# Performance work log

Hardware: AMD Instinct MI355X
Metric: run time of the kernel (lower is better)

## Reference

```python
import jax, jax.numpy as jnp
import numpy as np

NUM_HEADS = 8


def setup_inputs() -> dict:
    key = jax.random.key(0)
    ks = jax.random.split(key, 5)
    B, C, H, W = 2, 256, 64, 64
    # 0.02 scaling keeps logits in a sane range so softmax is not one-hot
    return {
        "x": jax.random.normal(ks[0], (B, C, H, W), dtype=jnp.float32),
        "w_qkv": jax.random.normal(ks[1], (3 * C, C), dtype=jnp.float32) * 0.02,
        "b_qkv": jax.random.normal(ks[2], (3 * C,), dtype=jnp.float32) * 0.02,
        "w_proj": jax.random.normal(ks[3], (C, C), dtype=jnp.float32) * 0.02,
        "b_proj": jax.random.normal(ks[4], (C,), dtype=jnp.float32) * 0.02,
    }


def reference(x, w_qkv, b_qkv, w_proj, b_proj):
    B, C, H, W = x.shape
    N = H * W
    h = NUM_HEADS
    d = C // h
    # 1x1 conv == per-pixel linear: (B,C,H,W) -> (B,3C,H,W)
    qkv = jnp.einsum('oc,bchw->bohw', w_qkv, x) + b_qkv[None, :, None, None]
    qkv = qkv.reshape(B, 3, h, d, N)
    # q,k,v: (B, h, N, d)
    q = jnp.swapaxes(qkv[:, 0], -2, -1)
    k = jnp.swapaxes(qkv[:, 1], -2, -1)
    v = jnp.swapaxes(qkv[:, 2], -2, -1)
    scale = d ** (-0.5)
    attn = jax.nn.softmax(jnp.einsum('bhnd,bhmd->bhnm', q, k) * scale, axis=-1)
    out = jnp.einsum('bhnm,bhmd->bhnd', attn, v)  # (B, h, N, d)
    # faithful to torch: transpose(1,2) -> (B,N,h,d), then row-major reshape to (B,C,H,W)
    out = jnp.swapaxes(out, 1, 2).reshape(B, C, H, W)
    out = jnp.einsum('oc,bchw->bohw', w_proj, out) + b_proj[None, :, None, None]
    return out
```

## Files before the change

### kernel.cpp

```cpp
#include <hip/hip_runtime.h>
#include <hip/hip_bf16.h>


typedef __bf16 bf16;
typedef __bf16 bf16x4 __attribute__((ext_vector_type(4)));
typedef __bf16 bf16x8 __attribute__((ext_vector_type(8)));
typedef float  f32x4  __attribute__((ext_vector_type(4)));
typedef short  s16x4  __attribute__((ext_vector_type(4)));

#if __has_builtin(__builtin_amdgcn_mfma_f32_16x16x16bf16_1k)
#define HAVE_MFMA16 1
#endif

#if __has_builtin(__builtin_amdgcn_exp2f)
#define EXP2(x) __builtin_amdgcn_exp2f(x)
#else
#define EXP2(x) exp2f(x)
#endif

#define NS 4096
#define QSCALE (0.17677669529663687f * 1.4426950408889634f)

static __device__ inline unsigned pack2(float a, float b) {
  union { bf16 h[2]; unsigned u; } v;
  v.h[0] = (bf16)a; v.h[1] = (bf16)b;
  return v.u;
}

__global__ __launch_bounds__(256) void qkv_fused(
    const float* __restrict__ x, const float* __restrict__ w,
    const float* __restrict__ bias,
    bf16* __restrict__ qbuf, bf16* __restrict__ kbuf, bf16* __restrict__ vbuf)
{
  __shared__ bf16 As[64 * 264];
  __shared__ bf16 Bs[64 * 264];
  const int n0 = blockIdx.x * 64, o0 = blockIdx.y * 64, b = blockIdx.z;
  const int t = threadIdx.x;
  const int wv = t >> 6, L = t & 63, quad = L >> 4, lb = L & 15;

  {
    unsigned* A32 = (unsigned*)As;
    const int nj = (t & 15) * 4;
#pragma unroll
    for (int p = 0; p < 8; p++) {
      const int c = p * 32 + (t >> 4) * 2;
      const float* xr = x + ((size_t)(b * 256 + c)) * NS + n0 + nj;
      f32x4 va = *(const f32x4*)xr;
      f32x4 vb = *(const f32x4*)(xr + NS);
#pragma unroll
      for (int i = 0; i < 4; i++)
        A32[(nj + i) * 132 + (c >> 1)] = pack2(va[i], vb[i]);
    }
  }
  {
    const int cj = (t & 15) * 16;
#pragma unroll
    for (int p = 0; p < 4; p++) {
      const int r = p * 16 + (t >> 4);
      const float* wr = w + (size_t)(o0 + r) * 256 + cj;
      f32x4 w0 = *(const f32x4*)wr,       w1 = *(const f32x4*)(wr + 4);
      f32x4 w2 = *(const f32x4*)(wr + 8), w3 = *(const f32x4*)(wr + 12);
      bf16x8 lo, hi;
#pragma unroll
      for (int i = 0; i < 4; i++) {
        lo[i] = (bf16)w0[i]; lo[4 + i] = (bf16)w1[i];
        hi[i] = (bf16)w2[i]; hi[4 + i] = (bf16)w3[i];
      }
      *(bf16x8*)&Bs[r * 264 + cj] = lo;
      *(bf16x8*)&Bs[r * 264 + cj + 8] = hi;
    }
  }
  __syncthreads();

  f32x4 acc[4] = {};
#pragma unroll
  for (int ks = 0; ks < 8; ks++) {
    const bf16x8 bfr = *(const bf16x8*)&Bs[(wv * 16 + lb) * 264 + ks * 32 + quad * 8];
#pragma unroll
    for (int a = 0; a < 4; a++) {
      const bf16x8 afr = *(const bf16x8*)&As[(a * 16 + lb) * 264 + ks * 32 + quad * 8];
      acc[a] = __builtin_amdgcn_mfma_f32_16x16x32_bf16(afr, bfr, acc[a], 0, 0, 0);
    }
  }

  const int comp = o0 >> 8;
  const int o = o0 + wv * 16 + lb;
  const float bv = bias[o];
  if (comp < 2) {
    bf16* dst = (comp == 0) ? qbuf : kbuf;
    const float sc = (comp == 0) ? QSCALE : 1.0f;
    const int hh = (o & 255) >> 5, dd = o & 31;
    const size_t base = ((size_t)b * 8 + hh) * NS;
#pragma unroll
    for (int a = 0; a < 4; a++)
#pragma unroll
      for (int r = 0; r < 4; r++) {
        const int n = n0 + a * 16 + quad * 4 + r;
        dst[(base + n) * 32 + dd] = (bf16)((acc[a][r] + bv) * sc);
      }
  } else {
    __syncthreads();
    bf16* Vt2 = As;
#pragma unroll
    for (int a = 0; a < 4; a++)
#pragma unroll
      for (int r = 0; r < 4; r++)
        Vt2[(wv * 16 + lb) * 72 + a * 16 + quad * 4 + r] = (bf16)(acc[a][r] + bv);
    __syncthreads();
    const int row = t & 63;
    const int o2 = o0 + row;
    const int hh2 = (o2 & 255) >> 5, dd2 = o2 & 31;
    const int hc = (t >> 6) * 16;
    bf16x8 v0 = *(const bf16x8*)&Vt2[row * 72 + hc];
    bf16x8 v1 = *(const bf16x8*)&Vt2[row * 72 + hc + 8];
    bf16* vd = vbuf + (((size_t)b * 8 + hh2) * 32 + dd2) * NS + n0 + hc;
    *(bf16x8*)vd = v0;
    *(bf16x8*)(vd + 8) = v1;
  }
}

__global__ __launch_bounds__(256) void attn_kernel(
    const bf16* __restrict__ qbuf, const bf16* __restrict__ kbuf,
    const bf16* __restrict__ vbuf, bf16* __restrict__ abuf)
{
  __shared__ bf16 Ks[2][64 * 40];
  __shared__ bf16 Vts[2][32 * 80];
#ifndef HAVE_MFMA16
  __shared__ bf16 Ps[4][16 * 72];
#endif

  const int qb = blockIdx.x;
  const int bh = blockIdx.y;
  const bf16* Q  = qbuf + (size_t)bh * NS * 32;
  const bf16* K  = kbuf + (size_t)bh * NS * 32;
  const bf16* Vt = vbuf + (size_t)bh * 32 * NS;

  const int t = threadIdx.x;
  const int wv = t >> 6, L = t & 63, quad = L >> 4, lb = L & 15;
  const int qrow = qb * 64 + wv * 16;

  const bf16x8 qfrag = *(const bf16x8*)(Q + (size_t)(qrow + lb) * 32 + quad * 8);

  const int ki = t >> 2, kj = (t & 3) * 8;
  const int vr = t >> 3, vc = (t & 7) * 8;
  const bf16* Kg = K + (size_t)ki * 32 + kj;
  const bf16* Vg = Vt + (size_t)vr * NS + vc;

  bf16x8 kreg = *(const bf16x8*)Kg;
  bf16x8 vreg = *(const bf16x8*)Vg;

  f32x4 oacc0 = {0.f, 0.f, 0.f, 0.f};
  f32x4 oacc1 = {0.f, 0.f, 0.f, 0.f};
  f32x4 oacc2 = {0.f, 0.f, 0.f, 0.f};
  const f32x4 zero4 = {0.f, 0.f, 0.f, 0.f};
#ifdef HAVE_MFMA16
  const s16x4 ones = {(short)0x3F80, (short)0x3F80, (short)0x3F80, (short)0x3F80};
#else
  float l_i = 0.f;
#endif

#pragma unroll 2
  for (int kt = 0; kt < 64; kt++) {
    const int buf = kt & 1;
    *(bf16x8*)&Ks[buf][ki * 40 + kj] = kreg;
    *(bf16x8*)&Vts[buf][vr * 80 + vc] = vreg;
    __syncthreads();
    if (kt < 63) {
      kreg = *(const bf16x8*)(Kg + (size_t)(kt + 1) * 64 * 32);
      vreg = *(const bf16x8*)(Vg + (size_t)(kt + 1) * 64);
    }

    f32x4 st[4];
#pragma unroll
    for (int bi = 0; bi < 4; bi++) {
      const bf16x8 kf = *(const bf16x8*)&Ks[buf][(bi * 16 + lb) * 40 + quad * 8];
      st[bi] = __builtin_amdgcn_mfma_f32_16x16x32_bf16(kf, qfrag, zero4, 0, 0, 0);
    }

#pragma unroll
    for (int bi = 0; bi < 4; bi++)
#pragma unroll
      for (int r = 0; r < 4; r++) st[bi][r] = EXP2(st[bi][r]);

#ifdef HAVE_MFMA16
#pragma unroll
    for (int bi = 0; bi < 4; bi++) {
      bf16x4 pb;
#pragma unroll
      for (int r = 0; r < 4; r++) pb[r] = (bf16)st[bi][r];
      const s16x4 pf = __builtin_bit_cast(s16x4, pb);
      const s16x4 vf0 = __builtin_bit_cast(s16x4,
          *(const bf16x4*)&Vts[buf][lb * 80 + bi * 16 + quad * 4]);
      const s16x4 vf1 = __builtin_bit_cast(s16x4,
          *(const bf16x4*)&Vts[buf][(16 + lb) * 80 + bi * 16 + quad * 4]);
      oacc0 = __builtin_amdgcn_mfma_f32_16x16x16bf16_1k(pf, vf0, oacc0, 0, 0, 0);
      oacc1 = __builtin_amdgcn_mfma_f32_16x16x16bf16_1k(pf, vf1, oacc1, 0, 0, 0);
      oacc2 = __builtin_amdgcn_mfma_f32_16x16x16bf16_1k(pf, ones, oacc2, 0, 0, 0);
    }
#else
    {
      float ls = 0.f;
#pragma unroll
      for (int bi = 0; bi < 4; bi++)
#pragma unroll
        for (int r = 0; r < 4; r++) ls += st[bi][r];
      l_i += ls;
      bf16* P = &Ps[wv][0];
#pragma unroll
      for (int bi = 0; bi < 4; bi++) {
        bf16x4 pk;
#pragma unroll
        for (int r = 0; r < 4; r++) pk[r] = (bf16)st[bi][r];
        *(bf16x4*)&P[lb * 72 + bi * 16 + quad * 4] = pk;
      }
#pragma unroll
      for (int ch = 0; ch < 2; ch++) {
        const bf16x8 pf  = *(const bf16x8*)&P[lb * 72 + ch * 32 + quad * 8];
        const bf16x8 vf0 = *(const bf16x8*)&Vts[buf][lb * 80 + ch * 32 + quad * 8];
        const bf16x8 vf1 = *(const bf16x8*)&Vts[buf][(16 + lb) * 80 + ch * 32 + quad * 8];
        oacc0 = __builtin_amdgcn_mfma_f32_16x16x32_bf16(pf, vf0, oacc0, 0, 0, 0);
        oacc1 = __builtin_amdgcn_mfma_f32_16x16x32_bf16(pf, vf1, oacc1, 0, 0, 0);
      }
      __syncthreads();
    }
#endif
  }

  const int b_ = bh >> 3;
  const int hh = bh & 7;
#ifndef HAVE_MFMA16
  float lf = l_i;
  lf += __shfl_xor(lf, 16);
  lf += __shfl_xor(lf, 32);
#endif
#pragma unroll
  for (int r = 0; r < 4; r++) {
#ifdef HAVE_MFMA16
    const float lr = oacc2[r];
#else
    const float lr = __shfl(lf, (quad << 4) | (quad * 4 + r));
#endif
#if __has_builtin(__builtin_amdgcn_rcpf)
    const float inv = __builtin_amdgcn_rcpf(lr);
#else
    const float inv = 1.0f / lr;
#endif
    const int n = qrow + quad * 4 + r;
    bf16* dst = abuf + ((size_t)b_ * NS + n) * 256 + hh * 32;
    dst[lb]      = (bf16)(oacc0[r] * inv);
    dst[16 + lb] = (bf16)(oacc1[r] * inv);
  }
}

__global__ __launch_bounds__(256) void proj_fused(
    const bf16* __restrict__ abuf, const float* __restrict__ w,
    const float* __restrict__ bias, float* __restrict__ out)
{
  __shared__ bf16 As[64 * 264];
  __shared__ bf16 Bs[64 * 264];
  const int ch0 = blockIdx.x * 64, o0 = blockIdx.y * 64;
  const int z = blockIdx.z, b = z >> 4, sHi = z & 15;
  const int t = threadIdx.x;
  const int wv = t >> 6, L = t & 63, quad = L >> 4, lb = L & 15;

  {
    const int cj = (t & 15) * 16;
#pragma unroll
    for (int p = 0; p < 4; p++) {
      const int r = p * 16 + (t >> 4);
      const float* wr = w + (size_t)(o0 + r) * 256 + cj;
      f32x4 w0 = *(const f32x4*)wr,       w1 = *(const f32x4*)(wr + 4);
      f32x4 w2 = *(const f32x4*)(wr + 8), w3 = *(const f32x4*)(wr + 12);
      bf16x8 lo, hi;
#pragma unroll
      for (int i = 0; i < 4; i++) {
        lo[i] = (bf16)w0[i]; lo[4 + i] = (bf16)w1[i];
        hi[i] = (bf16)w2[i]; hi[4 + i] = (bf16)w3[i];
      }
      *(bf16x8*)&As[r * 264 + cj] = lo;
      *(bf16x8*)&As[r * 264 + cj + 8] = hi;
    }
  }
  {
    const int chj = (t & 7) * 8;
#pragma unroll
    for (int p = 0; p < 8; p++) {
      const int c = p * 32 + (t >> 3);
      bf16x8 v = *(const bf16x8*)(abuf +
          ((size_t)b * NS + (size_t)c * 16 + sHi) * 256 + ch0 + chj);
#pragma unroll
      for (int i = 0; i < 8; i++) Bs[(chj + i) * 264 + c] = v[i];
    }
  }
  __syncthreads();

  f32x4 acc[4] = {};
#pragma unroll
  for (int ks = 0; ks < 8; ks++) {
    const bf16x8 bfr = *(const bf16x8*)&Bs[(wv * 16 + lb) * 264 + ks * 32 + quad * 8];
#pragma unroll
    for (int a = 0; a < 4; a++) {
      const bf16x8 afr = *(const bf16x8*)&As[(a * 16 + lb) * 264 + ks * 32 + quad * 8];
      acc[a] = __builtin_amdgcn_mfma_f32_16x16x32_bf16(afr, bfr, acc[a], 0, 0, 0);
    }
  }

  const int ch = ch0 + wv * 16 + lb;
#pragma unroll
  for (int a = 0; a < 4; a++)
#pragma unroll
    for (int r = 0; r < 4; r++) {
      const int o = o0 + a * 16 + quad * 4 + r;
      out[((size_t)b * 256 + o) * NS + sHi * 256 + ch] = acc[a][r] + bias[o];
    }
}

extern "C" void kernel_launch(void* const* d_in, const int* in_sizes, int n_in,
                              void* d_out, int out_size, void* d_ws, size_t ws_size,
                              hipStream_t stream) {
  const float* x      = (const float*)d_in[0];
  const float* w_qkv  = (const float*)d_in[1];
  const float* b_qkv  = (const float*)d_in[2];
  const float* w_proj = (const float*)d_in[3];
  const float* b_proj = (const float*)d_in[4];
  float* out = (float*)d_out;

  char* ws = (char*)d_ws;
  const size_t MB = 1024 * 1024;
  bf16* qbuf = (bf16*)(ws);
  bf16* kbuf = (bf16*)(ws + 4 * MB);
  bf16* vbuf = (bf16*)(ws + 8 * MB);
  bf16* abuf = (bf16*)(ws + 12 * MB);

  qkv_fused<<<dim3(64, 12, 2), 256, 0, stream>>>(x, w_qkv, b_qkv, qbuf, kbuf, vbuf);
  attn_kernel<<<dim3(64, 16), 256, 0, stream>>>(qbuf, kbuf, vbuf, abuf);
  proj_fused<<<dim3(4, 4, 32), 256, 0, stream>>>(abuf, w_proj, b_proj, out);
}
```

Before: 179.7 us.

## Double attention block to 128 query rows and split K/V staging across threads

The attention kernel now runs 512 threads (8 waves) per block covering 128 query rows, so each staged K/V tile is reused by twice as many waves and global K/V traffic per query is halved. Loading is split: the first 256 threads fetch K and the other 256 fetch V into a single combined shared buffer with a tighter V row stride. The grid halves to 32x16 blocks (512 blocks), which lowers the number of resident blocks and may reduce latency hiding. The non-MFMA16 fallback loses a trailing __syncthreads, which could introduce a shared-memory race there.

```diff
diff --git a/kernel.cpp b/kernel.cpp
--- a/kernel.cpp
+++ b/kernel.cpp
@@ -119,14 +119,17 @@
   }
 }
 
-__global__ __launch_bounds__(256) void attn_kernel(
+#define KS_OFF 0
+#define VT_OFF 2560
+#define KV_SZ  (2560 + 32 * 72)
+
+__global__ __launch_bounds__(512) void attn_kernel(
     const bf16* __restrict__ qbuf, const bf16* __restrict__ kbuf,
     const bf16* __restrict__ vbuf, bf16* __restrict__ abuf)
 {
-  __shared__ bf16 Ks[2][64 * 40];
-  __shared__ bf16 Vts[2][32 * 80];
+  __shared__ bf16 KV[2][KV_SZ];
 #ifndef HAVE_MFMA16
-  __shared__ bf16 Ps[4][16 * 72];
+  __shared__ bf16 Ps[8][16 * 72];
 #endif
 
   const int qb = blockIdx.x;
@@ -137,17 +140,19 @@
 
   const int t = threadIdx.x;
   const int wv = t >> 6, L = t & 63, quad = L >> 4, lb = L & 15;
-  const int qrow = qb * 64 + wv * 16;
+  const int qrow = qb * 128 + wv * 16;
 
   const bf16x8 qfrag = *(const bf16x8*)(Q + (size_t)(qrow + lb) * 32 + quad * 8);
 
-  const int ki = t >> 2, kj = (t & 3) * 8;
-  const int vr = t >> 3, vc = (t & 7) * 8;
-  const bf16* Kg = K + (size_t)ki * 32 + kj;
-  const bf16* Vg = Vt + (size_t)vr * NS + vc;
-
-  bf16x8 kreg = *(const bf16x8*)Kg;
-  bf16x8 vreg = *(const bf16x8*)Vg;
+  const int u = t & 255;
+  const bool kside = t < 256;
+  const int soff = kside ? ((u >> 2) * 40 + (u & 3) * 8)
+                         : (VT_OFF + (u >> 3) * 72 + (u & 7) * 8);
+  const bf16* gsrc = kside ? (K + (size_t)(u >> 2) * 32 + (u & 3) * 8)
+                           : (Vt + (size_t)(u >> 3) * NS + (u & 7) * 8);
+  const int gstep = kside ? 64 * 32 : 64;
+
+  bf16x8 reg = *(const bf16x8*)gsrc;
 
   f32x4 oacc0 = {0.f, 0.f, 0.f, 0.f};
   f32x4 oacc1 = {0.f, 0.f, 0.f, 0.f};
@@ -162,18 +167,14 @@
 #pragma unroll 2
   for (int kt = 0; kt < 64; kt++) {
     const int buf = kt & 1;
-    *(bf16x8*)&Ks[buf][ki * 40 + kj] = kreg;
-    *(bf16x8*)&Vts[buf][vr * 80 + vc] = vreg;
+    *(bf16x8*)&KV[buf][soff] = reg;
     __syncthreads();
-    if (kt < 63) {
-      kreg = *(const bf16x8*)(Kg + (size_t)(kt + 1) * 64 * 32);
-      vreg = *(const bf16x8*)(Vg + (size_t)(kt + 1) * 64);
-    }
+    if (kt < 63) reg = *(const bf16x8*)(gsrc + (size_t)(kt + 1) * gstep);
 
     f32x4 st[4];
 #pragma unroll
     for (int bi = 0; bi < 4; bi++) {
-      const bf16x8 kf = *(const bf16x8*)&Ks[buf][(bi * 16 + lb) * 40 + quad * 8];
+      const bf16x8 kf = *(const bf16x8*)&KV[buf][(bi * 16 + lb) * 40 + quad * 8];
       st[bi] = __builtin_amdgcn_mfma_f32_16x16x32_bf16(kf, qfrag, zero4, 0, 0, 0);
     }
 
@@ -190,9 +191,9 @@
       for (int r = 0; r < 4; r++) pb[r] = (bf16)st[bi][r];
       const s16x4 pf = __builtin_bit_cast(s16x4, pb);
       const s16x4 vf0 = __builtin_bit_cast(s16x4,
-          *(const bf16x4*)&Vts[buf][lb * 80 + bi * 16 + quad * 4]);
+          *(const bf16x4*)&KV[buf][VT_OFF + lb * 72 + bi * 16 + quad * 4]);
       const s16x4 vf1 = __builtin_bit_cast(s16x4,
-          *(const bf16x4*)&Vts[buf][(16 + lb) * 80 + bi * 16 + quad * 4]);
+          *(const bf16x4*)&KV[buf][VT_OFF + (16 + lb) * 72 + bi * 16 + quad * 4]);
       oacc0 = __builtin_amdgcn_mfma_f32_16x16x16bf16_1k(pf, vf0, oacc0, 0, 0, 0);
       oacc1 = __builtin_amdgcn_mfma_f32_16x16x16bf16_1k(pf, vf1, oacc1, 0, 0, 0);
       oacc2 = __builtin_amdgcn_mfma_f32_16x16x16bf16_1k(pf, ones, oacc2, 0, 0, 0);
@@ -216,12 +217,11 @@
 #pragma unroll
       for (int ch = 0; ch < 2; ch++) {
         const bf16x8 pf  = *(const bf16x8*)&P[lb * 72 + ch * 32 + quad * 8];
-        const bf16x8 vf0 = *(const bf16x8*)&Vts[buf][lb * 80 + ch * 32 + quad * 8];
-        const bf16x8 vf1 = *(const bf16x8*)&Vts[buf][(16 + lb) * 80 + ch * 32 + quad * 8];
+        const bf16x8 vf0 = *(const bf16x8*)&KV[buf][VT_OFF + lb * 72 + ch * 32 + quad * 8];
+        const bf16x8 vf1 = *(const bf16x8*)&KV[buf][VT_OFF + (16 + lb) * 72 + ch * 32 + quad * 8];
         oacc0 = __builtin_amdgcn_mfma_f32_16x16x32_bf16(pf, vf0, oacc0, 0, 0, 0);
         oacc1 = __builtin_amdgcn_mfma_f32_16x16x32_bf16(pf, vf1, oacc1, 0, 0, 0);
       }
-      __syncthreads();
     }
 #endif
   }
@@ -333,6 +333,6 @@
   bf16* abuf = (bf16*)(ws + 12 * MB);
 
   qkv_fused<<<dim3(64, 12, 2), 256, 0, stream>>>(x, w_qkv, b_qkv, qbuf, kbuf, vbuf);
-  attn_kernel<<<dim3(64, 16), 256, 0, stream>>>(qbuf, kbuf, vbuf, abuf);
+  attn_kernel<<<dim3(32, 16), 512, 0, stream>>>(qbuf, kbuf, vbuf, abuf);
   proj_fused<<<dim3(4, 4, 32), 256, 0, stream>>>(abuf, w_proj, b_proj, out);
 }
```

New measurement: 151.6 us. 15.6% less time.
